# Optimization experiments

Hardware: AMD Instinct MI355X
Metric: run time of the kernel (lower is better)

Reference implementation:

```python
import jax, jax.numpy as jnp
import numpy as np

R = 256   # resolution
C = 16    # n_chan
F = 8     # n_freq
N = 262144


def setup_inputs() -> dict:
    key = jax.random.key(0)
    k1, k2 = jax.random.split(key)
    coords = jax.random.uniform(k1, (N, 3), dtype=jnp.float32, minval=-1.0, maxval=1.0)
    grid = jax.random.normal(k2, (3, C * F, R, R), dtype=jnp.float32) * 0.1
    # matches torch init: linspace(0,1,C*F).reshape(-1,C).T.reshape(-1)
    freqs = jnp.linspace(0.0, 1.0, C * F, dtype=jnp.float32).reshape(-1, C).T.reshape(-1)
    return {"coords": coords, "grid": grid, "freqs": freqs}


def _reflect(x, size):
    # PyTorch grid_sample reflection padding, align_corners=True:
    # reflect unnormalized coords about [0, size-1], period 2*(size-1)
    span = size - 1
    m = 2 * span
    r = jnp.abs(x) % m
    return jnp.where(r > span, m - r, r)


def _grid_sample_plane(img, xy):
    # img: (CF, R, R); xy: (Npts, 2) normalized [-1,1], (x indexes W, y indexes H)
    ix = _reflect((xy[:, 0] + 1.0) * 0.5 * (R - 1), R)
    iy = _reflect((xy[:, 1] + 1.0) * 0.5 * (R - 1), R)
    x0f = jnp.floor(ix); y0f = jnp.floor(iy)
    wx = ix - x0f; wy = iy - y0f
    x0 = jnp.clip(x0f.astype(jnp.int32), 0, R - 1)
    x1 = jnp.clip(x0 + 1, 0, R - 1)
    y0 = jnp.clip(y0f.astype(jnp.int32), 0, R - 1)
    y1 = jnp.clip(y0 + 1, 0, R - 1)
    v00 = img[:, y0, x0]  # (CF, Npts)
    v01 = img[:, y0, x1]
    v10 = img[:, y1, x0]
    v11 = img[:, y1, x1]
    return (v00 * (1 - wx) * (1 - wy) + v01 * wx * (1 - wy)
            + v10 * (1 - wx) * wy + v11 * wx * wy)


def reference(coords, grid, freqs):
    n = coords.shape[0]
    # tri-plane sample coords: plane0 (y,z), plane1 (x,z), plane2 (x,y)
    xy = jnp.stack([coords[:, (1, 2)], coords[:, (0, 2)], coords[:, (0, 1)]], 0)  # (3,N,2)
    coefs = jax.vmap(_grid_sample_plane)(grid, xy)          # (3, CF, N)
    coefs = coefs.transpose(2, 1, 0).reshape(n, C, F, 3)    # (N, C, F, 3)
    # get_freqs(): 2**(clamp(freqs,0,1)*log2(R)) - 1
    fr = 2.0 ** (jnp.clip(freqs, 0.0, 1.0) * np.float32(np.log2(R))) - 1.0  # (CF,)
    pts = (coords + 1.0) * 0.5 * (R - 1)                    # (N, 3)
    phase = (jnp.pi / R) * (pts[:, None, None, :] + 0.5) * (fr.reshape(C, F)[None, :, :, None] + 0.5)
    basis = jnp.cos(phase)                                   # (N, C, F, 3)
    # einsum BCFT,BCFT->BCT then sum over T == sum over (F, T)
    return 2.0 * jnp.sum(coefs * basis, axis=(2, 3))         # (N, C)
```

## Files before the change

kernel.cpp:

```cpp
#include <hip/hip_runtime.h>

#define RES   256
#define NCH   128
#define NC    16
#define QG    32
#define NPK   64
#define NBINS 4096
#define TBLK  3072

typedef float  fx4 __attribute__((ext_vector_type(4)));

__device__ __forceinline__ unsigned int f32_to_bf16_rne(float f) {
    unsigned int u = __float_as_uint(f);
    return (u + 0x7FFFu + ((u >> 16) & 1u)) >> 16;
}
__device__ __forceinline__ float bf16_lo(unsigned int w) {
    return __uint_as_float(w << 16);
}
__device__ __forceinline__ float bf16_hi(unsigned int w) {
    return __uint_as_float(w & 0xFFFF0000u);
}
__device__ __forceinline__ float reflectf(float v) {
    float r = fabsf(v);
    r = fmodf(r, 510.0f);
    return (r > 255.0f) ? (510.0f - r) : r;
}
__device__ __forceinline__ unsigned spread3(unsigned v) {
    return (v & 1u) | ((v & 2u) << 2) | ((v & 4u) << 4) | ((v & 8u) << 6);
}
__device__ __forceinline__ int point_cell(const float* __restrict__ coords, int i) {
    const float r0 = reflectf((coords[3 * (size_t)i + 0] + 1.0f) * 127.5f);
    const float r1 = reflectf((coords[3 * (size_t)i + 1] + 1.0f) * 127.5f);
    const float r2 = reflectf((coords[3 * (size_t)i + 2] + 1.0f) * 127.5f);
    const unsigned cx = (unsigned)min(max((int)r0, 0), 255) >> 4;
    const unsigned cy = (unsigned)min(max((int)r1, 0), 255) >> 4;
    const unsigned cz = (unsigned)min(max((int)r2, 0), 255) >> 4;
    return (int)(spread3(cx) | (spread3(cy) << 1) | (spread3(cz) << 2));
}

__global__ __launch_bounds__(256) void fg_transpose_hist(
    const float* __restrict__ in, unsigned int* __restrict__ out,
    const float* __restrict__ coords, unsigned* __restrict__ hist, int n)
{
    __shared__ unsigned int tile[QG / 2][RES + 4];
    const int tid = threadIdx.x;
    const int qg = blockIdx.x;
    const int y  = blockIdx.y;
    const int p  = blockIdx.z;

    {
        const int bid = (p * RES + y) * 4 + qg;
        const int per = (n + TBLK - 1) / TBLK;
        const int s0 = bid * per;
        const int s1 = min(s0 + per, n);
        for (int k = s0 + tid; k < s1; k += 256)
            atomicAdd(&hist[point_cell(coords, k)], 1u);
    }

    const int q0 = qg * QG;
    const float* src = in + (((size_t)p * NCH + q0) * RES + y) * RES;
    #pragma unroll
    for (int it = 0; it < 4; ++it) {
        const int lin = it * 256 + tid;
        const int k   = lin >> 6;
        const int x4  = lin & 63;
        const fx4 a = __builtin_nontemporal_load(
            (const fx4*)(src + (size_t)(2 * k + 0) * (RES * RES) + x4 * 4));
        const fx4 b = __builtin_nontemporal_load(
            (const fx4*)(src + (size_t)(2 * k + 1) * (RES * RES) + x4 * 4));
        uint4 w;
        w.x = f32_to_bf16_rne(a.x) | (f32_to_bf16_rne(b.x) << 16);
        w.y = f32_to_bf16_rne(a.y) | (f32_to_bf16_rne(b.y) << 16);
        w.z = f32_to_bf16_rne(a.z) | (f32_to_bf16_rne(b.z) << 16);
        w.w = f32_to_bf16_rne(a.w) | (f32_to_bf16_rne(b.w) << 16);
        *(uint4*)&tile[k][x4 * 4] = w;
    }
    __syncthreads();
    unsigned int* dst = out + (((size_t)p * RES + y) * RES) * NPK + (q0 >> 1);
    #pragma unroll
    for (int it = 0; it < 4; ++it) {
        const int lin = it * 256 + tid;
        const int q4 = lin & 3;
        const int x  = lin >> 2;
        uint4 w;
        w.x = tile[4 * q4 + 0][x];
        w.y = tile[4 * q4 + 1][x];
        w.z = tile[4 * q4 + 2][x];
        w.w = tile[4 * q4 + 3][x];
        *(uint4*)&dst[(size_t)x * NPK + q4 * 4] = w;
    }
}

__global__ __launch_bounds__(256) void fg_scan(
    const unsigned* __restrict__ hist, unsigned* __restrict__ cursor,
    const float* __restrict__ freqs, float* __restrict__ frp)
{
    __shared__ unsigned wtot[4];
    const int t = threadIdx.x;
    const int lane = t & 63;
    const int wid = t >> 6;
    unsigned loc[16];
    unsigned sum = 0;
    #pragma unroll
    for (int k = 0; k < 16; ++k) { loc[k] = hist[t * 16 + k]; sum += loc[k]; }
    unsigned v = sum;
    #pragma unroll
    for (int off = 1; off < 64; off <<= 1) {
        unsigned u = __shfl_up(v, off);
        if (lane >= off) v += u;
    }
    if (lane == 63) wtot[wid] = v;
    __syncthreads();
    unsigned base = 0;
    #pragma unroll
    for (int w = 0; w < 4; ++w) base += (w < wid) ? wtot[w] : 0u;
    unsigned run = base + (v - sum);
    #pragma unroll
    for (int k = 0; k < 16; ++k) { cursor[t * 16 + k] = run; run += loc[k]; }
    if (t < 128) {
        const float f = fminf(fmaxf(freqs[t], 0.0f), 1.0f);
        frp[t] = __builtin_amdgcn_exp2f(f * 8.0f) - 0.5f;
    }
}

__global__ __launch_bounds__(256) void fg_scatter(
    const float* __restrict__ coords, unsigned* __restrict__ cursor,
    float4* __restrict__ rec, int n)
{
    const int i = blockIdx.x * 256 + threadIdx.x;
    if (i >= n) return;
    const float c0 = coords[3 * (size_t)i + 0];
    const float c1 = coords[3 * (size_t)i + 1];
    const float c2 = coords[3 * (size_t)i + 2];
    const float p0 = (c0 + 1.0f) * 127.5f;
    const float p1 = (c1 + 1.0f) * 127.5f;
    const float p2 = (c2 + 1.0f) * 127.5f;
    const float r0 = reflectf(p0);
    const float r1 = reflectf(p1);
    const float r2 = reflectf(p2);
    const unsigned cx = (unsigned)min(max((int)r0, 0), 255) >> 4;
    const unsigned cy = (unsigned)min(max((int)r1, 0), 255) >> 4;
    const unsigned cz = (unsigned)min(max((int)r2, 0), 255) >> 4;
    const int cell = (int)(spread3(cx) | (spread3(cy) << 1) | (spread3(cz) << 2));
    const unsigned pos = atomicAdd(&cursor[cell], 1u);
    rec[pos] = make_float4(p0, p1, p2, __uint_as_float((unsigned)i));
}

__global__ __launch_bounds__(256) void fg_main_bf16(
    const unsigned int* __restrict__ grid,
    const float* __restrict__ frp_in,
    const float4* __restrict__ rec,
    float* __restrict__ out, int n)
{
    const int t = threadIdx.x;
    const int c = t & 15;
    int b = blockIdx.x;
    {
        const int G = gridDim.x;
        const int chunk = G >> 3;
        const int lim = chunk << 3;
        if (b < lim) b = (b & 7) * chunk + (b >> 3);
    }
    const int slot = b * 16 + (t >> 4);
    if (slot >= n) return;
    const float4 r = rec[slot];
    const int i = (int)__float_as_uint(r.w);

    float frp[8];
    *(float4*)(frp + 0) = *(const float4*)(frp_in + c * 8 + 0);
    *(float4*)(frp + 4) = *(const float4*)(frp_in + c * 8 + 4);

    const float pts0 = r.x;
    const float pts1 = r.y;
    const float pts2 = r.z;

    float Aa[3], W00[3], W01[3], W10[3], W11[3];
    uint4 g[3][4];

    #pragma unroll
    for (int p = 0; p < 3; ++p) {
        const float sx = (p == 0) ? pts1 : pts0;
        const float sy = (p == 2) ? pts1 : pts2;
        const float pp = (p == 0) ? pts0 : ((p == 1) ? pts1 : pts2);

        const float ix = reflectf(sx);
        const float iy = reflectf(sy);
        const float x0f = floorf(ix), y0f = floorf(iy);
        const float wx = ix - x0f, wy = iy - y0f;
        int x0 = (int)x0f; x0 = min(max(x0, 0), RES - 1);
        int y0 = (int)y0f; y0 = min(max(y0, 0), RES - 1);
        const int x1 = min(x0 + 1, RES - 1);
        const int y1 = min(y0 + 1, RES - 1);
        W00[p] = (1.0f - wx) * (1.0f - wy);
        W01[p] = wx * (1.0f - wy);
        W10[p] = (1.0f - wx) * wy;
        W11[p] = wx * wy;
        Aa[p] = (pp + 0.5f) * (1.0f / 512.0f);

        const int rowbase = p * (RES * RES);
        const int o00 = (rowbase + y0 * RES + x0) * NPK + c * 4;
        const int o01 = (rowbase + y0 * RES + x1) * NPK + c * 4;
        const int o10 = (rowbase + y1 * RES + x0) * NPK + c * 4;
        const int o11 = (rowbase + y1 * RES + x1) * NPK + c * 4;
        g[p][0] = *(const uint4*)(grid + o00);
        g[p][1] = *(const uint4*)(grid + o01);
        g[p][2] = *(const uint4*)(grid + o10);
        g[p][3] = *(const uint4*)(grid + o11);
    }

    float acc = 0.0f;
    #pragma unroll
    for (int p = 0; p < 3; ++p) {
        const unsigned int w0[4] = {g[p][0].x, g[p][0].y, g[p][0].z, g[p][0].w};
        const unsigned int w1[4] = {g[p][1].x, g[p][1].y, g[p][1].z, g[p][1].w};
        const unsigned int w2[4] = {g[p][2].x, g[p][2].y, g[p][2].z, g[p][2].w};
        const unsigned int w3[4] = {g[p][3].x, g[p][3].y, g[p][3].z, g[p][3].w};
        const float w00 = W00[p], w01 = W01[p], w10 = W10[p], w11 = W11[p];
        const float A = Aa[p];

        #pragma unroll
        for (int jj = 0; jj < 4; ++jj) {
            const float clo = w00 * bf16_lo(w0[jj]) + w01 * bf16_lo(w1[jj])
                            + w10 * bf16_lo(w2[jj]) + w11 * bf16_lo(w3[jj]);
            const float chi = w00 * bf16_hi(w0[jj]) + w01 * bf16_hi(w1[jj])
                            + w10 * bf16_hi(w2[jj]) + w11 * bf16_hi(w3[jj]);
            const float rl = __builtin_amdgcn_fractf(A * frp[2 * jj + 0]);
            const float rh = __builtin_amdgcn_fractf(A * frp[2 * jj + 1]);
            acc += clo * __builtin_amdgcn_cosf(rl);
            acc += chi * __builtin_amdgcn_cosf(rh);
        }
    }

    __builtin_nontemporal_store(2.0f * acc, &out[(size_t)i * NC + c]);
}

__global__ __launch_bounds__(256) void fg_main_f32(
    const float* __restrict__ coords,
    const float* __restrict__ grid,
    const float* __restrict__ freqs,
    float* __restrict__ out, int n)
{
    const int t = threadIdx.x;
    const int c = t & 15;
    const int i = blockIdx.x * 16 + (t >> 4);
    if (i >= n) return;

    float frp[8];
    #pragma unroll
    for (int j = 0; j < 8; ++j) {
        float f = fminf(fmaxf(freqs[c * 8 + j], 0.0f), 1.0f);
        frp[j] = __builtin_amdgcn_exp2f(f * 8.0f) - 0.5f;
    }
    const float c0 = coords[3 * (size_t)i + 0];
    const float c1 = coords[3 * (size_t)i + 1];
    const float c2 = coords[3 * (size_t)i + 2];
    const float pts0 = (c0 + 1.0f) * 127.5f;
    const float pts1 = (c1 + 1.0f) * 127.5f;
    const float pts2 = (c2 + 1.0f) * 127.5f;
    float acc = 0.0f;
    #pragma unroll
    for (int p = 0; p < 3; ++p) {
        const float sx = (p == 0) ? pts1 : pts0;
        const float sy = (p == 2) ? pts1 : pts2;
        const float pp = (p == 0) ? pts0 : ((p == 1) ? pts1 : pts2);
        const float ix = reflectf(sx);
        const float iy = reflectf(sy);
        const float x0f = floorf(ix), y0f = floorf(iy);
        const float wx = ix - x0f, wy = iy - y0f;
        int x0 = (int)x0f; x0 = min(max(x0, 0), RES - 1);
        int y0 = (int)y0f; y0 = min(max(y0, 0), RES - 1);
        const int x1 = min(x0 + 1, RES - 1);
        const int y1 = min(y0 + 1, RES - 1);
        const float w00 = (1.0f - wx) * (1.0f - wy);
        const float w01 = wx * (1.0f - wy);
        const float w10 = (1.0f - wx) * wy;
        const float w11 = wx * wy;
        const float A = (pp + 0.5f) * (1.0f / 512.0f);
        const size_t plane = (size_t)p * NCH * RES * RES;
        const int o00 = y0 * RES + x0, o01 = y0 * RES + x1;
        const int o10 = y1 * RES + x0, o11 = y1 * RES + x1;
        #pragma unroll
        for (int j = 0; j < 8; ++j) {
            const float* gq = grid + plane + (size_t)(c * 8 + j) * (RES * RES);
            const float coef = w00 * gq[o00] + w01 * gq[o01]
                             + w10 * gq[o10] + w11 * gq[o11];
            const float rr = __builtin_amdgcn_fractf(A * frp[j]);
            acc += coef * __builtin_amdgcn_cosf(rr);
        }
    }
    out[(size_t)i * NC + c] = 2.0f * acc;
}

extern "C" void kernel_launch(void* const* d_in, const int* in_sizes, int n_in,
                              void* d_out, int out_size, void* d_ws, size_t ws_size,
                              hipStream_t stream)
{
    const float* coords = (const float*)d_in[0];
    const float* grid   = (const float*)d_in[1];
    const float* freqs  = (const float*)d_in[2];
    float* out = (float*)d_out;
    const int n = in_sizes[0] / 3;

    const size_t gridT_b  = (size_t)3 * RES * RES * NPK * sizeof(unsigned);
    const size_t hist_b   = (size_t)NBINS * sizeof(unsigned);
    const size_t frp_b    = 128 * sizeof(float);
    const size_t rec_b    = (size_t)n * sizeof(float4);
    const size_t need = gridT_b + 2 * hist_b + frp_b + rec_b;

    const int blocks = (n + 15) / 16;

    if (ws_size >= need) {
        char* ws = (char*)d_ws;
        unsigned* gridT  = (unsigned*)ws;                 ws += gridT_b;
        unsigned* hist   = (unsigned*)ws;                 ws += hist_b;
        unsigned* cursor = (unsigned*)ws;                 ws += hist_b;
        float*    frp    = (float*)ws;                    ws += frp_b;
        float4*   rec    = (float4*)ws;

        (void)hipMemsetAsync(hist, 0, hist_b, stream);
        hipLaunchKernelGGL(fg_transpose_hist, dim3(4, RES, 3), dim3(256), 0, stream,
                           grid, gridT, coords, hist, n);
        hipLaunchKernelGGL(fg_scan, dim3(1), dim3(256), 0, stream,
                           hist, cursor, freqs, frp);
        hipLaunchKernelGGL(fg_scatter, dim3((n + 255) / 256), dim3(256), 0, stream,
                           coords, cursor, rec, n);
        hipLaunchKernelGGL(fg_main_bf16, dim3(blocks), dim3(256), 0, stream,
                           gridT, frp, rec, out, n);
    } else {
        hipLaunchKernelGGL(fg_main_f32, dim3(blocks), dim3(256), 0, stream,
                           coords, grid, freqs, out, n);
    }
}
```

Baseline: 240.1 us.

## Process two points per thread in main kernel to batch gather loads

Each thread in the bf16 main kernel now handles two sorted points, issuing all 24 grid gathers for both before doing either point's interpolation and cosine work. This raises memory-level parallelism per wave so gather latency is better hidden, and halves the block count. The cost is roughly doubled register use, which may lower occupancy. Separately, the transpose kernel's nontemporal loads are replaced with plain loads.

```diff
diff --git a/kernel.cpp b/kernel.cpp
--- a/kernel.cpp
+++ b/kernel.cpp
@@ -7,8 +7,6 @@
 #define NPK   64
 #define NBINS 4096
 #define TBLK  3072
-
-typedef float  fx4 __attribute__((ext_vector_type(4)));
 
 __device__ __forceinline__ unsigned int f32_to_bf16_rne(float f) {
     unsigned int u = __float_as_uint(f);
@@ -64,10 +62,8 @@
         const int lin = it * 256 + tid;
         const int k   = lin >> 6;
         const int x4  = lin & 63;
-        const fx4 a = __builtin_nontemporal_load(
-            (const fx4*)(src + (size_t)(2 * k + 0) * (RES * RES) + x4 * 4));
-        const fx4 b = __builtin_nontemporal_load(
-            (const fx4*)(src + (size_t)(2 * k + 1) * (RES * RES) + x4 * 4));
+        const float4 a = *(const float4*)(src + (size_t)(2 * k + 0) * (RES * RES) + x4 * 4);
+        const float4 b = *(const float4*)(src + (size_t)(2 * k + 1) * (RES * RES) + x4 * 4);
         uint4 w;
         w.x = f32_to_bf16_rne(a.x) | (f32_to_bf16_rne(b.x) << 16);
         w.y = f32_to_bf16_rne(a.y) | (f32_to_bf16_rne(b.y) << 16);
@@ -146,43 +142,18 @@
     rec[pos] = make_float4(p0, p1, p2, __uint_as_float((unsigned)i));
 }
 
-__global__ __launch_bounds__(256) void fg_main_bf16(
-    const unsigned int* __restrict__ grid,
-    const float* __restrict__ frp_in,
-    const float4* __restrict__ rec,
-    float* __restrict__ out, int n)
-{
-    const int t = threadIdx.x;
-    const int c = t & 15;
-    int b = blockIdx.x;
-    {
-        const int G = gridDim.x;
-        const int chunk = G >> 3;
-        const int lim = chunk << 3;
-        if (b < lim) b = (b & 7) * chunk + (b >> 3);
-    }
-    const int slot = b * 16 + (t >> 4);
-    if (slot >= n) return;
-    const float4 r = rec[slot];
-    const int i = (int)__float_as_uint(r.w);
-
-    float frp[8];
-    *(float4*)(frp + 0) = *(const float4*)(frp_in + c * 8 + 0);
-    *(float4*)(frp + 4) = *(const float4*)(frp_in + c * 8 + 4);
-
-    const float pts0 = r.x;
-    const float pts1 = r.y;
-    const float pts2 = r.z;
-
-    float Aa[3], W00[3], W01[3], W10[3], W11[3];
-    uint4 g[3][4];
-
+struct PtSetup {
+    float A[3], W00[3], W01[3], W10[3], W11[3];
+    int   off[3][4];
+};
+
+__device__ __forceinline__ void pt_setup(const float4 r, const int c, PtSetup& s) {
+    const float pts0 = r.x, pts1 = r.y, pts2 = r.z;
     #pragma unroll
     for (int p = 0; p < 3; ++p) {
         const float sx = (p == 0) ? pts1 : pts0;
         const float sy = (p == 2) ? pts1 : pts2;
         const float pp = (p == 0) ? pts0 : ((p == 1) ? pts1 : pts2);
-
         const float ix = reflectf(sx);
         const float iy = reflectf(sy);
         const float x0f = floorf(ix), y0f = floorf(iy);
@@ -191,23 +162,21 @@
         int y0 = (int)y0f; y0 = min(max(y0, 0), RES - 1);
         const int x1 = min(x0 + 1, RES - 1);
         const int y1 = min(y0 + 1, RES - 1);
-        W00[p] = (1.0f - wx) * (1.0f - wy);
-        W01[p] = wx * (1.0f - wy);
-        W10[p] = (1.0f - wx) * wy;
-        W11[p] = wx * wy;
-        Aa[p] = (pp + 0.5f) * (1.0f / 512.0f);
-
+        s.W00[p] = (1.0f - wx) * (1.0f - wy);
+        s.W01[p] = wx * (1.0f - wy);
+        s.W10[p] = (1.0f - wx) * wy;
+        s.W11[p] = wx * wy;
+        s.A[p] = (pp + 0.5f) * (1.0f / 512.0f);
         const int rowbase = p * (RES * RES);
-        const int o00 = (rowbase + y0 * RES + x0) * NPK + c * 4;
-        const int o01 = (rowbase + y0 * RES + x1) * NPK + c * 4;
-        const int o10 = (rowbase + y1 * RES + x0) * NPK + c * 4;
-        const int o11 = (rowbase + y1 * RES + x1) * NPK + c * 4;
-        g[p][0] = *(const uint4*)(grid + o00);
-        g[p][1] = *(const uint4*)(grid + o01);
-        g[p][2] = *(const uint4*)(grid + o10);
-        g[p][3] = *(const uint4*)(grid + o11);
-    }
-
+        s.off[p][0] = (rowbase + y0 * RES + x0) * NPK + c * 4;
+        s.off[p][1] = (rowbase + y0 * RES + x1) * NPK + c * 4;
+        s.off[p][2] = (rowbase + y1 * RES + x0) * NPK + c * 4;
+        s.off[p][3] = (rowbase + y1 * RES + x1) * NPK + c * 4;
+    }
+}
+
+__device__ __forceinline__ float pt_consume(const PtSetup& s, const uint4 g[3][4],
+                                            const float* __restrict__ frp) {
     float acc = 0.0f;
     #pragma unroll
     for (int p = 0; p < 3; ++p) {
@@ -215,9 +184,8 @@
         const unsigned int w1[4] = {g[p][1].x, g[p][1].y, g[p][1].z, g[p][1].w};
         const unsigned int w2[4] = {g[p][2].x, g[p][2].y, g[p][2].z, g[p][2].w};
         const unsigned int w3[4] = {g[p][3].x, g[p][3].y, g[p][3].z, g[p][3].w};
-        const float w00 = W00[p], w01 = W01[p], w10 = W10[p], w11 = W11[p];
-        const float A = Aa[p];
-
+        const float w00 = s.W00[p], w01 = s.W01[p], w10 = s.W10[p], w11 = s.W11[p];
+        const float A = s.A[p];
         #pragma unroll
         for (int jj = 0; jj < 4; ++jj) {
             const float clo = w00 * bf16_lo(w0[jj]) + w01 * bf16_lo(w1[jj])
@@ -230,8 +198,62 @@
             acc += chi * __builtin_amdgcn_cosf(rh);
         }
     }
-
-    __builtin_nontemporal_store(2.0f * acc, &out[(size_t)i * NC + c]);
+    return acc;
+}
+
+__global__ __launch_bounds__(256) void fg_main_bf16(
+    const unsigned int* __restrict__ grid,
+    const float* __restrict__ frp_in,
+    const float4* __restrict__ rec,
+    float* __restrict__ out, int n)
+{
+    const int t = threadIdx.x;
+    const int c = t & 15;
+    int b = blockIdx.x;
+    {
+        const int G = gridDim.x;
+        const int chunk = G >> 3;
+        const int lim = chunk << 3;
+        if (b < lim) b = (b & 7) * chunk + (b >> 3);
+    }
+    const int slotA = b * 32 + (t >> 4);
+    const int slotB = slotA + 16;
+    if (slotA >= n) return;
+    const bool hasB = (slotB < n);
+
+    const float4 rA = rec[slotA];
+    const float4 rB = rec[hasB ? slotB : slotA];
+    const int iA = (int)__float_as_uint(rA.w);
+    const int iB = (int)__float_as_uint(rB.w);
+
+    float frp[8];
+    *(float4*)(frp + 0) = *(const float4*)(frp_in + c * 8 + 0);
+    *(float4*)(frp + 4) = *(const float4*)(frp_in + c * 8 + 4);
+
+    PtSetup sA, sB;
+    pt_setup(rA, c, sA);
+    pt_setup(rB, c, sB);
+
+    uint4 gA[3][4], gB[3][4];
+    #pragma unroll
+    for (int p = 0; p < 3; ++p) {
+        #pragma unroll
+        for (int q = 0; q < 4; ++q)
+            gA[p][q] = *(const uint4*)(grid + sA.off[p][q]);
+    }
+    #pragma unroll
+    for (int p = 0; p < 3; ++p) {
+        #pragma unroll
+        for (int q = 0; q < 4; ++q)
+            gB[p][q] = *(const uint4*)(grid + sB.off[p][q]);
+    }
+
+    const float accA = pt_consume(sA, gA, frp);
+    __builtin_nontemporal_store(2.0f * accA, &out[(size_t)iA * NC + c]);
+
+    const float accB = pt_consume(sB, gB, frp);
+    if (hasB)
+        __builtin_nontemporal_store(2.0f * accB, &out[(size_t)iB * NC + c]);
 }
 
 __global__ __launch_bounds__(256) void fg_main_f32(
@@ -307,8 +329,6 @@
     const size_t rec_b    = (size_t)n * sizeof(float4);
     const size_t need = gridT_b + 2 * hist_b + frp_b + rec_b;
 
-    const int blocks = (n + 15) / 16;
-
     if (ws_size >= need) {
         char* ws = (char*)d_ws;
         unsigned* gridT  = (unsigned*)ws;                 ws += gridT_b;
@@ -324,9 +344,11 @@
                            hist, cursor, freqs, frp);
         hipLaunchKernelGGL(fg_scatter, dim3((n + 255) / 256), dim3(256), 0, stream,
                            coords, cursor, rec, n);
-        hipLaunchKernelGGL(fg_main_bf16, dim3(blocks), dim3(256), 0, stream,
+        const int blocks2 = (n + 31) / 32;
+        hipLaunchKernelGGL(fg_main_bf16, dim3(blocks2), dim3(256), 0, stream,
                            gridT, frp, rec, out, n);
     } else {
+        const int blocks = (n + 15) / 16;
         hipLaunchKernelGGL(fg_main_f32, dim3(blocks), dim3(256), 0, stream,
                            coords, grid, freqs, out, n);
     }
```

New measurement: 246.8 us. +2.8%, slower.

## Precompute per-plane sample offsets and weights in scatter, vectorize main math

Applied to the files above, without the earlier changes.

The scatter kernel now computes, for each point and plane, the reflected coordinates, bilinear fractions, cosine phase scale and a packed gather offset with neighbour-valid flags. It writes these as three float4 records plus a separate index array. The main kernel no longer does reflect/fmod/clamp work, so it is left with loads, bf16 unpacking and float2-vectorized FMA and cosine accumulation. In exchange the per-point record grows from 16 to 52 bytes, adding memory traffic in scatter and main. The transpose loads also drop their nontemporal hint.

```diff
diff --git a/kernel.cpp b/kernel.cpp
--- a/kernel.cpp
+++ b/kernel.cpp
@@ -8,7 +8,7 @@
 #define NBINS 4096
 #define TBLK  3072
 
-typedef float  fx4 __attribute__((ext_vector_type(4)));
+typedef float fx2 __attribute__((ext_vector_type(2)));
 
 __device__ __forceinline__ unsigned int f32_to_bf16_rne(float f) {
     unsigned int u = __float_as_uint(f);
@@ -64,10 +64,8 @@
         const int lin = it * 256 + tid;
         const int k   = lin >> 6;
         const int x4  = lin & 63;
-        const fx4 a = __builtin_nontemporal_load(
-            (const fx4*)(src + (size_t)(2 * k + 0) * (RES * RES) + x4 * 4));
-        const fx4 b = __builtin_nontemporal_load(
-            (const fx4*)(src + (size_t)(2 * k + 1) * (RES * RES) + x4 * 4));
+        const float4 a = *(const float4*)(src + (size_t)(2 * k + 0) * (RES * RES) + x4 * 4);
+        const float4 b = *(const float4*)(src + (size_t)(2 * k + 1) * (RES * RES) + x4 * 4);
         uint4 w;
         w.x = f32_to_bf16_rne(a.x) | (f32_to_bf16_rne(b.x) << 16);
         w.y = f32_to_bf16_rne(a.y) | (f32_to_bf16_rne(b.y) << 16);
@@ -125,7 +123,7 @@
 
 __global__ __launch_bounds__(256) void fg_scatter(
     const float* __restrict__ coords, unsigned* __restrict__ cursor,
-    float4* __restrict__ rec, int n)
+    float4* __restrict__ recP, unsigned* __restrict__ idx, int n)
 {
     const int i = blockIdx.x * 256 + threadIdx.x;
     if (i >= n) return;
@@ -143,13 +141,30 @@
     const unsigned cz = (unsigned)min(max((int)r2, 0), 255) >> 4;
     const int cell = (int)(spread3(cx) | (spread3(cy) << 1) | (spread3(cz) << 2));
     const unsigned pos = atomicAdd(&cursor[cell], 1u);
-    rec[pos] = make_float4(p0, p1, p2, __uint_as_float((unsigned)i));
+
+    #pragma unroll
+    for (int p = 0; p < 3; ++p) {
+        const float ix = (p == 0) ? r1 : r0;
+        const float iy = (p == 2) ? r1 : r2;
+        const float pp = (p == 0) ? p0 : ((p == 1) ? p1 : p2);
+        const float x0f = floorf(ix), y0f = floorf(iy);
+        const float wx = ix - x0f, wy = iy - y0f;
+        const int x0 = min(max((int)x0f, 0), RES - 1);
+        const int y0 = min(max((int)y0f, 0), RES - 1);
+        unsigned ob = (unsigned)(((p << 16) | (y0 << 8) | x0) << 6);
+        if (x0 < RES - 1) ob |= (1u << 24);
+        if (y0 < RES - 1) ob |= (1u << 25);
+        const float A = (pp + 0.5f) * (1.0f / 512.0f);
+        recP[(size_t)pos * 3 + p] = make_float4(A, wx, wy, __uint_as_float(ob));
+    }
+    idx[pos] = (unsigned)i;
 }
 
 __global__ __launch_bounds__(256) void fg_main_bf16(
     const unsigned int* __restrict__ grid,
     const float* __restrict__ frp_in,
-    const float4* __restrict__ rec,
+    const float4* __restrict__ recP,
+    const unsigned* __restrict__ idx,
     float* __restrict__ out, int n)
 {
     const int t = threadIdx.x;
@@ -163,75 +178,70 @@
     }
     const int slot = b * 16 + (t >> 4);
     if (slot >= n) return;
-    const float4 r = rec[slot];
-    const int i = (int)__float_as_uint(r.w);
-
-    float frp[8];
-    *(float4*)(frp + 0) = *(const float4*)(frp_in + c * 8 + 0);
-    *(float4*)(frp + 4) = *(const float4*)(frp_in + c * 8 + 4);
-
-    const float pts0 = r.x;
-    const float pts1 = r.y;
-    const float pts2 = r.z;
-
-    float Aa[3], W00[3], W01[3], W10[3], W11[3];
+
+    float4 P[3];
+    P[0] = recP[(size_t)slot * 3 + 0];
+    P[1] = recP[(size_t)slot * 3 + 1];
+    P[2] = recP[(size_t)slot * 3 + 2];
+    const unsigned i = idx[slot];
+
+    fx2 frpv[4];
+    {
+        float frp[8];
+        *(float4*)(frp + 0) = *(const float4*)(frp_in + c * 8 + 0);
+        *(float4*)(frp + 4) = *(const float4*)(frp_in + c * 8 + 4);
+        #pragma unroll
+        for (int jj = 0; jj < 4; ++jj) {
+            frpv[jj].x = frp[2 * jj + 0];
+            frpv[jj].y = frp[2 * jj + 1];
+        }
+    }
+
+    const int c4 = c * 4;
     uint4 g[3][4];
-
     #pragma unroll
     for (int p = 0; p < 3; ++p) {
-        const float sx = (p == 0) ? pts1 : pts0;
-        const float sy = (p == 2) ? pts1 : pts2;
-        const float pp = (p == 0) ? pts0 : ((p == 1) ? pts1 : pts2);
-
-        const float ix = reflectf(sx);
-        const float iy = reflectf(sy);
-        const float x0f = floorf(ix), y0f = floorf(iy);
-        const float wx = ix - x0f, wy = iy - y0f;
-        int x0 = (int)x0f; x0 = min(max(x0, 0), RES - 1);
-        int y0 = (int)y0f; y0 = min(max(y0, 0), RES - 1);
-        const int x1 = min(x0 + 1, RES - 1);
-        const int y1 = min(y0 + 1, RES - 1);
-        W00[p] = (1.0f - wx) * (1.0f - wy);
-        W01[p] = wx * (1.0f - wy);
-        W10[p] = (1.0f - wx) * wy;
-        W11[p] = wx * wy;
-        Aa[p] = (pp + 0.5f) * (1.0f / 512.0f);
-
-        const int rowbase = p * (RES * RES);
-        const int o00 = (rowbase + y0 * RES + x0) * NPK + c * 4;
-        const int o01 = (rowbase + y0 * RES + x1) * NPK + c * 4;
-        const int o10 = (rowbase + y1 * RES + x0) * NPK + c * 4;
-        const int o11 = (rowbase + y1 * RES + x1) * NPK + c * 4;
-        g[p][0] = *(const uint4*)(grid + o00);
-        g[p][1] = *(const uint4*)(grid + o01);
-        g[p][2] = *(const uint4*)(grid + o10);
-        g[p][3] = *(const uint4*)(grid + o11);
-    }
-
-    float acc = 0.0f;
+        const unsigned bits = __float_as_uint(P[p].w);
+        const int base = (int)(bits & 0x00FFFFFFu) + c4;
+        const int dx = (int)((bits >> 18) & 64u);
+        const int dy = (int)((bits >> 11) & 16384u);
+        g[p][0] = *(const uint4*)(grid + base);
+        g[p][1] = *(const uint4*)(grid + base + dx);
+        g[p][2] = *(const uint4*)(grid + base + dy);
+        g[p][3] = *(const uint4*)(grid + base + dx + dy);
+    }
+
+    fx2 acc2 = {0.0f, 0.0f};
     #pragma unroll
     for (int p = 0; p < 3; ++p) {
+        const float wx = P[p].y, wy = P[p].z;
+        const float u = 1.0f - wx, v = 1.0f - wy;
+        const float w00 = u * v,  w01 = wx * v;
+        const float w10 = u * wy, w11 = wx * wy;
+        const float A = P[p].x;
         const unsigned int w0[4] = {g[p][0].x, g[p][0].y, g[p][0].z, g[p][0].w};
         const unsigned int w1[4] = {g[p][1].x, g[p][1].y, g[p][1].z, g[p][1].w};
         const unsigned int w2[4] = {g[p][2].x, g[p][2].y, g[p][2].z, g[p][2].w};
         const unsigned int w3[4] = {g[p][3].x, g[p][3].y, g[p][3].z, g[p][3].w};
-        const float w00 = W00[p], w01 = W01[p], w10 = W10[p], w11 = W11[p];
-        const float A = Aa[p];
 
         #pragma unroll
         for (int jj = 0; jj < 4; ++jj) {
-            const float clo = w00 * bf16_lo(w0[jj]) + w01 * bf16_lo(w1[jj])
-                            + w10 * bf16_lo(w2[jj]) + w11 * bf16_lo(w3[jj]);
-            const float chi = w00 * bf16_hi(w0[jj]) + w01 * bf16_hi(w1[jj])
-                            + w10 * bf16_hi(w2[jj]) + w11 * bf16_hi(w3[jj]);
-            const float rl = __builtin_amdgcn_fractf(A * frp[2 * jj + 0]);
-            const float rh = __builtin_amdgcn_fractf(A * frp[2 * jj + 1]);
-            acc += clo * __builtin_amdgcn_cosf(rl);
-            acc += chi * __builtin_amdgcn_cosf(rh);
+            fx2 v0; v0.x = bf16_lo(w0[jj]); v0.y = bf16_hi(w0[jj]);
+            fx2 v1; v1.x = bf16_lo(w1[jj]); v1.y = bf16_hi(w1[jj]);
+            fx2 v2; v2.x = bf16_lo(w2[jj]); v2.y = bf16_hi(w2[jj]);
+            fx2 v3; v3.x = bf16_lo(w3[jj]); v3.y = bf16_hi(w3[jj]);
+            const fx2 cf = w00 * v0 + w01 * v1 + w10 * v2 + w11 * v3;
+            fx2 ph = A * frpv[jj];
+            ph.x = __builtin_amdgcn_fractf(ph.x);
+            ph.y = __builtin_amdgcn_fractf(ph.y);
+            fx2 cs;
+            cs.x = __builtin_amdgcn_cosf(ph.x);
+            cs.y = __builtin_amdgcn_cosf(ph.y);
+            acc2 += cf * cs;
         }
     }
 
-    __builtin_nontemporal_store(2.0f * acc, &out[(size_t)i * NC + c]);
+    __builtin_nontemporal_store(2.0f * (acc2.x + acc2.y), &out[(size_t)i * NC + c]);
 }
 
 __global__ __launch_bounds__(256) void fg_main_f32(
@@ -304,10 +314,9 @@
     const size_t gridT_b  = (size_t)3 * RES * RES * NPK * sizeof(unsigned);
     const size_t hist_b   = (size_t)NBINS * sizeof(unsigned);
     const size_t frp_b    = 128 * sizeof(float);
-    const size_t rec_b    = (size_t)n * sizeof(float4);
-    const size_t need = gridT_b + 2 * hist_b + frp_b + rec_b;
-
-    const int blocks = (n + 15) / 16;
+    const size_t recP_b   = (size_t)n * 3 * sizeof(float4);
+    const size_t idx_b    = (size_t)((n + 3) & ~3) * sizeof(unsigned);
+    const size_t need = gridT_b + 2 * hist_b + frp_b + recP_b + idx_b;
 
     if (ws_size >= need) {
         char* ws = (char*)d_ws;
@@ -315,7 +324,8 @@
         unsigned* hist   = (unsigned*)ws;                 ws += hist_b;
         unsigned* cursor = (unsigned*)ws;                 ws += hist_b;
         float*    frp    = (float*)ws;                    ws += frp_b;
-        float4*   rec    = (float4*)ws;
+        float4*   recP   = (float4*)ws;                   ws += recP_b;
+        unsigned* idxb   = (unsigned*)ws;
 
         (void)hipMemsetAsync(hist, 0, hist_b, stream);
         hipLaunchKernelGGL(fg_transpose_hist, dim3(4, RES, 3), dim3(256), 0, stream,
@@ -323,10 +333,12 @@
         hipLaunchKernelGGL(fg_scan, dim3(1), dim3(256), 0, stream,
                            hist, cursor, freqs, frp);
         hipLaunchKernelGGL(fg_scatter, dim3((n + 255) / 256), dim3(256), 0, stream,
-                           coords, cursor, rec, n);
+                           coords, cursor, recP, idxb, n);
+        const int blocks = (n + 15) / 16;
         hipLaunchKernelGGL(fg_main_bf16, dim3(blocks), dim3(256), 0, stream,
-                           gridT, frp, rec, out, n);
+                           gridT, frp, recP, idxb, out, n);
     } else {
+        const int blocks = (n + 15) / 16;
         hipLaunchKernelGGL(fg_main_f32, dim3(blocks), dim3(256), 0, stream,
                            coords, grid, freqs, out, n);
     }
```

New measurement: 244.0 us. Within noise of the previous version (+1.6%).

## Drop spatial binning of points and sample directly in input order

Applied to the files above, without the earlier changes.

Removes the histogram, scan and scatter passes that sorted points into Morton-ordered 16^3 cells, and removes the block-index swizzle. The main kernel now reads coords directly and handles points in their original order. The frequency precompute moves into the first block of the transpose kernel. This saves three launches, a memset, the atomics and the record buffer traffic, but gives up the gather locality on the bf16 grid that sorting provided for random coordinates.

```diff
diff --git a/kernel.cpp b/kernel.cpp
--- a/kernel.cpp
+++ b/kernel.cpp
@@ -5,10 +5,8 @@
 #define NC    16
 #define QG    32
 #define NPK   64
-#define NBINS 4096
-#define TBLK  3072
-
-typedef float  fx4 __attribute__((ext_vector_type(4)));
+
+typedef float fx4 __attribute__((ext_vector_type(4)));
 
 __device__ __forceinline__ unsigned int f32_to_bf16_rne(float f) {
     unsigned int u = __float_as_uint(f);
@@ -25,22 +23,10 @@
     r = fmodf(r, 510.0f);
     return (r > 255.0f) ? (510.0f - r) : r;
 }
-__device__ __forceinline__ unsigned spread3(unsigned v) {
-    return (v & 1u) | ((v & 2u) << 2) | ((v & 4u) << 4) | ((v & 8u) << 6);
-}
-__device__ __forceinline__ int point_cell(const float* __restrict__ coords, int i) {
-    const float r0 = reflectf((coords[3 * (size_t)i + 0] + 1.0f) * 127.5f);
-    const float r1 = reflectf((coords[3 * (size_t)i + 1] + 1.0f) * 127.5f);
-    const float r2 = reflectf((coords[3 * (size_t)i + 2] + 1.0f) * 127.5f);
-    const unsigned cx = (unsigned)min(max((int)r0, 0), 255) >> 4;
-    const unsigned cy = (unsigned)min(max((int)r1, 0), 255) >> 4;
-    const unsigned cz = (unsigned)min(max((int)r2, 0), 255) >> 4;
-    return (int)(spread3(cx) | (spread3(cy) << 1) | (spread3(cz) << 2));
-}
-
-__global__ __launch_bounds__(256) void fg_transpose_hist(
+
+__global__ __launch_bounds__(256) void fg_transpose(
     const float* __restrict__ in, unsigned int* __restrict__ out,
-    const float* __restrict__ coords, unsigned* __restrict__ hist, int n)
+    const float* __restrict__ freqs, float* __restrict__ frp)
 {
     __shared__ unsigned int tile[QG / 2][RES + 4];
     const int tid = threadIdx.x;
@@ -48,13 +34,9 @@
     const int y  = blockIdx.y;
     const int p  = blockIdx.z;
 
-    {
-        const int bid = (p * RES + y) * 4 + qg;
-        const int per = (n + TBLK - 1) / TBLK;
-        const int s0 = bid * per;
-        const int s1 = min(s0 + per, n);
-        for (int k = s0 + tid; k < s1; k += 256)
-            atomicAdd(&hist[point_cell(coords, k)], 1u);
+    if (qg == 0 && y == 0 && p == 0 && tid < 128) {
+        const float f = fminf(fmaxf(freqs[tid], 0.0f), 1.0f);
+        frp[tid] = __builtin_amdgcn_exp2f(f * 8.0f) - 0.5f;
     }
 
     const int q0 = qg * QG;
@@ -91,88 +73,27 @@
     }
 }
 
-__global__ __launch_bounds__(256) void fg_scan(
-    const unsigned* __restrict__ hist, unsigned* __restrict__ cursor,
-    const float* __restrict__ freqs, float* __restrict__ frp)
-{
-    __shared__ unsigned wtot[4];
+__global__ __launch_bounds__(256) void fg_main_bf16(
+    const unsigned int* __restrict__ grid,
+    const float* __restrict__ frp_in,
+    const float* __restrict__ coords,
+    float* __restrict__ out, int n)
+{
     const int t = threadIdx.x;
-    const int lane = t & 63;
-    const int wid = t >> 6;
-    unsigned loc[16];
-    unsigned sum = 0;
-    #pragma unroll
-    for (int k = 0; k < 16; ++k) { loc[k] = hist[t * 16 + k]; sum += loc[k]; }
-    unsigned v = sum;
-    #pragma unroll
-    for (int off = 1; off < 64; off <<= 1) {
-        unsigned u = __shfl_up(v, off);
-        if (lane >= off) v += u;
-    }
-    if (lane == 63) wtot[wid] = v;
-    __syncthreads();
-    unsigned base = 0;
-    #pragma unroll
-    for (int w = 0; w < 4; ++w) base += (w < wid) ? wtot[w] : 0u;
-    unsigned run = base + (v - sum);
-    #pragma unroll
-    for (int k = 0; k < 16; ++k) { cursor[t * 16 + k] = run; run += loc[k]; }
-    if (t < 128) {
-        const float f = fminf(fmaxf(freqs[t], 0.0f), 1.0f);
-        frp[t] = __builtin_amdgcn_exp2f(f * 8.0f) - 0.5f;
-    }
-}
-
-__global__ __launch_bounds__(256) void fg_scatter(
-    const float* __restrict__ coords, unsigned* __restrict__ cursor,
-    float4* __restrict__ rec, int n)
-{
-    const int i = blockIdx.x * 256 + threadIdx.x;
+    const int c = t & 15;
+    const int i = blockIdx.x * 16 + (t >> 4);
     if (i >= n) return;
+
     const float c0 = coords[3 * (size_t)i + 0];
     const float c1 = coords[3 * (size_t)i + 1];
     const float c2 = coords[3 * (size_t)i + 2];
-    const float p0 = (c0 + 1.0f) * 127.5f;
-    const float p1 = (c1 + 1.0f) * 127.5f;
-    const float p2 = (c2 + 1.0f) * 127.5f;
-    const float r0 = reflectf(p0);
-    const float r1 = reflectf(p1);
-    const float r2 = reflectf(p2);
-    const unsigned cx = (unsigned)min(max((int)r0, 0), 255) >> 4;
-    const unsigned cy = (unsigned)min(max((int)r1, 0), 255) >> 4;
-    const unsigned cz = (unsigned)min(max((int)r2, 0), 255) >> 4;
-    const int cell = (int)(spread3(cx) | (spread3(cy) << 1) | (spread3(cz) << 2));
-    const unsigned pos = atomicAdd(&cursor[cell], 1u);
-    rec[pos] = make_float4(p0, p1, p2, __uint_as_float((unsigned)i));
-}
-
-__global__ __launch_bounds__(256) void fg_main_bf16(
-    const unsigned int* __restrict__ grid,
-    const float* __restrict__ frp_in,
-    const float4* __restrict__ rec,
-    float* __restrict__ out, int n)
-{
-    const int t = threadIdx.x;
-    const int c = t & 15;
-    int b = blockIdx.x;
-    {
-        const int G = gridDim.x;
-        const int chunk = G >> 3;
-        const int lim = chunk << 3;
-        if (b < lim) b = (b & 7) * chunk + (b >> 3);
-    }
-    const int slot = b * 16 + (t >> 4);
-    if (slot >= n) return;
-    const float4 r = rec[slot];
-    const int i = (int)__float_as_uint(r.w);
+    const float pts0 = (c0 + 1.0f) * 127.5f;
+    const float pts1 = (c1 + 1.0f) * 127.5f;
+    const float pts2 = (c2 + 1.0f) * 127.5f;
 
     float frp[8];
     *(float4*)(frp + 0) = *(const float4*)(frp_in + c * 8 + 0);
     *(float4*)(frp + 4) = *(const float4*)(frp_in + c * 8 + 4);
-
-    const float pts0 = r.x;
-    const float pts1 = r.y;
-    const float pts2 = r.z;
 
     float Aa[3], W00[3], W01[3], W10[3], W11[3];
     uint4 g[3][4];
@@ -302,30 +223,20 @@
     const int n = in_sizes[0] / 3;
 
     const size_t gridT_b  = (size_t)3 * RES * RES * NPK * sizeof(unsigned);
-    const size_t hist_b   = (size_t)NBINS * sizeof(unsigned);
     const size_t frp_b    = 128 * sizeof(float);
-    const size_t rec_b    = (size_t)n * sizeof(float4);
-    const size_t need = gridT_b + 2 * hist_b + frp_b + rec_b;
+    const size_t need = gridT_b + frp_b;
 
     const int blocks = (n + 15) / 16;
 
     if (ws_size >= need) {
         char* ws = (char*)d_ws;
-        unsigned* gridT  = (unsigned*)ws;                 ws += gridT_b;
-        unsigned* hist   = (unsigned*)ws;                 ws += hist_b;
-        unsigned* cursor = (unsigned*)ws;                 ws += hist_b;
-        float*    frp    = (float*)ws;                    ws += frp_b;
-        float4*   rec    = (float4*)ws;
-
-        (void)hipMemsetAsync(hist, 0, hist_b, stream);
-        hipLaunchKernelGGL(fg_transpose_hist, dim3(4, RES, 3), dim3(256), 0, stream,
-                           grid, gridT, coords, hist, n);
-        hipLaunchKernelGGL(fg_scan, dim3(1), dim3(256), 0, stream,
-                           hist, cursor, freqs, frp);
-        hipLaunchKernelGGL(fg_scatter, dim3((n + 255) / 256), dim3(256), 0, stream,
-                           coords, cursor, rec, n);
+        unsigned* gridT = (unsigned*)ws;                  ws += gridT_b;
+        float*    frp   = (float*)ws;
+
+        hipLaunchKernelGGL(fg_transpose, dim3(4, RES, 3), dim3(256), 0, stream,
+                           grid, gridT, freqs, frp);
         hipLaunchKernelGGL(fg_main_bf16, dim3(blocks), dim3(256), 0, stream,
-                           gridT, frp, rec, out, n);
+                           gridT, frp, coords, out, n);
     } else {
         hipLaunchKernelGGL(fg_main_f32, dim3(blocks), dim3(256), 0, stream,
                            coords, grid, freqs, out, n);
```

Result: slower. 257.7 us (+7.3%).
